# Performance work log

Measured on AMD Instinct MI355X. Metric: run time of the kernel, lower is better.

The kernel has to match this reference:

```python
import jax, jax.numpy as jnp
import numpy as np

BATCH = 256
SEQ_LEN = 96
PRED_LEN = 96
ENC_IN = 321
D_MODEL = 512


def setup_inputs() -> dict:
    key = jax.random.key(0)
    ks = jax.random.split(key, 7)
    s = 1.0 / np.sqrt(D_MODEL)
    x_enc = jax.random.normal(ks[0], (BATCH, SEQ_LEN, ENC_IN), jnp.float32)
    Wih = jax.random.uniform(ks[1], (4 * D_MODEL, ENC_IN), jnp.float32, -s, s)
    Whh = jax.random.uniform(ks[2], (4 * D_MODEL, D_MODEL), jnp.float32, -s, s)
    bih = jax.random.uniform(ks[3], (4 * D_MODEL,), jnp.float32, -s, s)
    bhh = jax.random.uniform(ks[4], (4 * D_MODEL,), jnp.float32, -s, s)
    Wp = jax.random.uniform(ks[5], (ENC_IN, D_MODEL), jnp.float32, -s, s)
    bp = jax.random.uniform(ks[6], (ENC_IN,), jnp.float32, -s, s)
    return {"x_enc": x_enc, "Wih": Wih, "Whh": Whh, "bih": bih, "bhh": bhh, "Wp": Wp, "bp": bp}


def _lstm_step(h, c, xt, Wih, Whh, bih, bhh):
    # PyTorch LSTM gate layout: [i, f, g, o]
    g = xt @ Wih.T + h @ Whh.T + (bih + bhh)  # (B, 4*D)
    i, f, gg, o = jnp.split(g, 4, axis=-1)
    c = jax.nn.sigmoid(f) * c + jax.nn.sigmoid(i) * jnp.tanh(gg)
    h = jax.nn.sigmoid(o) * jnp.tanh(c)
    return h, c


def reference(x_enc, Wih, Whh, bih, bhh, Wp, bp):
    # Instance norm over time (use_norm=True); means detached as in torch
    means = jax.lax.stop_gradient(jnp.mean(x_enc, axis=1, keepdims=True))
    xc = x_enc - means
    stdev = jnp.sqrt(jnp.var(xc, axis=1, keepdims=True) + 1e-5)
    x = xc / stdev

    B = x.shape[0]
    h0 = jnp.zeros((B, D_MODEL), x.dtype)
    c0 = jnp.zeros((B, D_MODEL), x.dtype)

    def enc_step(carry, xt):
        h, c = carry
        h, c = _lstm_step(h, c, xt, Wih, Whh, bih, bhh)
        return (h, c), None

    (h, c), _ = jax.lax.scan(enc_step, (h0, c0), jnp.swapaxes(x, 0, 1))

    def dec_step(carry, _):
        h, c = carry
        y = h @ Wp.T + bp          # (B, ENC_IN) decoded from hidden
        h, c = _lstm_step(h, c, y, Wih, Whh, bih, bhh)
        return (h, c), y

    _, ys = jax.lax.scan(dec_step, (h, c), None, length=PRED_LEN)
    dec_out = jnp.swapaxes(ys, 0, 1)  # (B, PRED_LEN, ENC_IN)

    dec_out = dec_out * stdev[:, 0:1, :] + means[:, 0:1, :]
    return dec_out
```

## Files before the change

kernel.cpp:

```cpp
#include <hip/hip_runtime.h>
#include <hip/hip_bf16.h>
#include <math.h>

#define BB 256
#define TT 96
#define PP 96
#define CC 321
#define CP 352
#define DD 512
#define GG 2048
#define NSTEPS 191

typedef __attribute__((ext_vector_type(8))) short bf16x8;
typedef __attribute__((ext_vector_type(4))) float f32x4;
typedef __hip_bfloat16 bf16;
typedef unsigned long long u64;

__global__ void norm_kernel(const float* __restrict__ x, float* __restrict__ meanp,
                            float* __restrict__ stdp, bf16* __restrict__ xn) {
    int g = blockIdx.x * 256 + threadIdx.x;
    if (g >= BB * CC) return;
    int b = g / CC, c = g % CC;
    const float* xp = x + b * TT * CC + c;
    float s = 0.f;
    for (int t = 0; t < TT; ++t) s += xp[t * CC];
    float mu = s * (1.f / TT);
    float v = 0.f;
    for (int t = 0; t < TT; ++t) { float d0 = xp[t * CC] - mu; v += d0 * d0; }
    float sd = sqrtf(v * (1.f / TT) + 1e-5f);
    float rs = 1.f / sd;
    meanp[g] = mu;
    stdp[g] = sd;
    for (int t = 0; t < TT; ++t)
        xn[(t * BB + b) * CP + c] = __float2bfloat16((xp[t * CC] - mu) * rs);
}

__global__ void cast_pad_kernel(const float* __restrict__ src, bf16* __restrict__ dst,
                                int rows, int cols, int ldd) {
    int i = blockIdx.x * 256 + threadIdx.x;
    if (i >= rows * cols) return;
    int r = i / cols, c = i % cols;
    dst[r * ldd + c] = __float2bfloat16(src[i]);
}

__global__ void transpose_wp_kernel(const float* __restrict__ wp, bf16* __restrict__ wpt) {
    int i = blockIdx.x * 256 + threadIdx.x;
    if (i >= DD * CC) return;
    int d = i / CC, c = i % CC;
    wpt[d * CP + c] = __float2bfloat16(wp[c * DD + d]);
}

__global__ void bias_kernel(const float* __restrict__ Wih, const float* __restrict__ bih,
                            const float* __restrict__ bhh, const float* __restrict__ bp,
                            float* __restrict__ bsum, float* __restrict__ beff) {
    int j = blockIdx.x * 256 + threadIdx.x;
    if (j >= GG) return;
    float s = bih[j] + bhh[j];
    float acc = 0.f;
    const float* w = Wih + j * CC;
    for (int c = 0; c < CC; ++c) acc += w[c] * bp[c];
    bsum[j] = s;
    beff[j] = s + acc;
}

__device__ __forceinline__ void gemm_core_64x64(const bf16* A, int lda, const bf16* Bt,
                                                int ldb, int K, int m0, int n0,
                                                f32x4 acc[4]) {
    __shared__ unsigned short As[64][40];
    __shared__ unsigned short Bs[64][40];
    int tid = threadIdx.x;
    int w = tid >> 6, lane = tid & 63;
    int quad = lane >> 4, col = lane & 15;
    int lr = tid >> 2, lc = (tid & 3) * 8;
    for (int k0 = 0; k0 < K; k0 += 32) {
        __syncthreads();
        *(uint4*)&As[lr][lc] = *(const uint4*)&A[(size_t)(m0 + lr) * lda + k0 + lc];
        *(uint4*)&Bs[lr][lc] = *(const uint4*)&Bt[(size_t)(n0 + lr) * ldb + k0 + lc];
        __syncthreads();
        bf16x8 a = *(const bf16x8*)&As[w * 16 + col][quad * 8];
#pragma unroll
        for (int nt = 0; nt < 4; ++nt) {
            bf16x8 bfr = *(const bf16x8*)&Bs[nt * 16 + col][quad * 8];
            acc[nt] = __builtin_amdgcn_mfma_f32_16x16x32_bf16(a, bfr, acc[nt], 0, 0, 0);
        }
    }
}

__global__ void weff_kernel(const bf16* __restrict__ WihP, const bf16* __restrict__ WpTP,
                            const float* __restrict__ Whh, bf16* __restrict__ WeffP) {
    f32x4 acc[4] = {{0,0,0,0},{0,0,0,0},{0,0,0,0},{0,0,0,0}};
    int m0 = blockIdx.y * 64, n0 = blockIdx.x * 64;
    gemm_core_64x64(WihP, CP, WpTP, CP, CP, m0, n0, acc);
    int tid = threadIdx.x, w = tid >> 6, lane = tid & 63;
    int quad = lane >> 4, col = lane & 15;
#pragma unroll
    for (int nt = 0; nt < 4; ++nt)
#pragma unroll
        for (int r = 0; r < 4; ++r) {
            int j = m0 + w * 16 + quad * 4 + r;
            int d = n0 + nt * 16 + col;
            WeffP[j * DD + d] = __float2bfloat16(acc[nt][r] + Whh[j * DD + d]);
        }
}

__global__ void proj_kernel(const bf16* __restrict__ Hdec, const bf16* __restrict__ WpP,
                            const float* __restrict__ bp, const float* __restrict__ stdp,
                            const float* __restrict__ meanp, float* __restrict__ out) {
    f32x4 acc[4] = {{0,0,0,0},{0,0,0,0},{0,0,0,0},{0,0,0,0}};
    int m0 = blockIdx.x * 64, n0 = blockIdx.y * 64;
    gemm_core_64x64(Hdec, DD, WpP, DD, DD, m0, n0, acc);
    int tid = threadIdx.x, w = tid >> 6, lane = tid & 63;
    int quad = lane >> 4, col = lane & 15;
#pragma unroll
    for (int nt = 0; nt < 4; ++nt) {
        int c = n0 + nt * 16 + col;
        if (c >= CC) continue;
        float bpc = bp[c];
#pragma unroll
        for (int r = 0; r < 4; ++r) {
            int row = m0 + w * 16 + quad * 4 + r;
            int t = row >> 8, b = row & 255;
            float y = acc[nt][r] + bpc;
            int sc = b * CC + c;
            out[(b * PP + t) * CC + c] = y * stdp[sc] + meanp[sc];
        }
    }
}

__global__ __launch_bounds__(128, 1) void lstm_persistent(
        const bf16* __restrict__ xn,
        const bf16* __restrict__ WihP,
        const bf16* __restrict__ WhhP,
        const bf16* __restrict__ WeffP,
        const float* __restrict__ bsum, const float* __restrict__ beff,
        bf16* __restrict__ hA, bf16* __restrict__ hB,
        bf16* __restrict__ Hdec,
        unsigned int* __restrict__ bar) {
    __shared__ unsigned short Whs[4 * 16 * 16 * 32];
    __shared__ unsigned short Wxs[4 * 11 * 16 * 32];

    const int tid = threadIdx.x;
    const int w = tid >> 6, lane = tid & 63;
    const int quad = lane >> 4, col = lane & 15;
    const int dt = blockIdx.x & 31;
    const int bt = blockIdx.x >> 5;
    const int d0 = dt * 16;
    const int b0 = bt * 32;
    const int batch = b0 + w * 16 + col;

    for (int i = tid; i < 64 * 44; i += 128) {
        int row = i / 44, c8 = i % 44;
        int gt = row >> 4, cl = row & 15;
        int ki = c8 >> 2, q = c8 & 3;
        *(uint4*)&Wxs[((gt * 11 + ki) * 16 + cl) * 32 + q * 8] =
            *((const uint4*)(WihP + (size_t)(gt * DD + d0 + cl) * CP) + c8);
    }
    for (int i = tid; i < 64 * 64; i += 128) {
        int row = i >> 6, c8 = i & 63;
        int gt = row >> 4, cl = row & 15;
        int ki = c8 >> 2, q = c8 & 3;
        *(uint4*)&Whs[((gt * 16 + ki) * 16 + cl) * 32 + q * 8] =
            *((const uint4*)(WhhP + (size_t)(gt * DD + d0 + cl) * DD) + c8);
    }
    __syncthreads();

    float creg[4] = {0.f, 0.f, 0.f, 0.f};
    float bs_[16], be_[16];
#pragma unroll
    for (int g4 = 0; g4 < 16; ++g4) {
        int gt = g4 >> 2, r = g4 & 3;
        bs_[g4] = bsum[gt * DD + d0 + quad * 4 + r];
        be_[g4] = beff[gt * DD + d0 + quad * 4 + r];
    }

    unsigned int gen = 0;

    for (int s = 0; s < NSTEPS; ++s) {
        const bool enc = (s < TT);
        const bf16* h_in;
        bf16* h_out;
        if (enc) {
            h_in  = (s & 1) ? hB : hA;
            h_out = (s == TT - 1) ? Hdec : ((s & 1) ? hA : hB);
        } else {
            int td = s - TT;
            h_in  = Hdec + (size_t)td * BB * DD;
            h_out = Hdec + (size_t)(td + 1) * BB * DD;
        }

        if (s == TT) {
            for (int i = tid; i < 64 * 64; i += 128) {
                int row = i >> 6, c8 = i & 63;
                int gt = row >> 4, cl = row & 15;
                int ki = c8 >> 2, q = c8 & 3;
                *(uint4*)&Whs[((gt * 16 + ki) * 16 + cl) * 32 + q * 8] =
                    *((const uint4*)(WeffP + (size_t)(gt * DD + d0 + cl) * DD) + c8);
            }
            __syncthreads();
        }

        f32x4 acc[4] = {{0,0,0,0},{0,0,0,0},{0,0,0,0},{0,0,0,0}};

        u64 hf[32];
        {
            u64* hp = (u64*)(h_in + (size_t)batch * DD);
#pragma unroll
            for (int ki = 0; ki < 16; ++ki) {
                hf[2 * ki] = __hip_atomic_load(&hp[ki * 8 + quad * 2],
                                               __ATOMIC_RELAXED, __HIP_MEMORY_SCOPE_AGENT);
                hf[2 * ki + 1] = __hip_atomic_load(&hp[ki * 8 + quad * 2 + 1],
                                                   __ATOMIC_RELAXED, __HIP_MEMORY_SCOPE_AGENT);
            }
        }

        if (enc) {
            uint4 xf[11];
            const uint4* xp = (const uint4*)(xn + (size_t)(s * BB + batch) * CP) + quad;
#pragma unroll
            for (int ki = 0; ki < 11; ++ki) xf[ki] = xp[ki * 4];
#pragma unroll
            for (int ki = 0; ki < 11; ++ki) {
                bf16x8 xv = *(bf16x8*)&xf[ki];
#pragma unroll
                for (int gt = 0; gt < 4; ++gt) {
                    bf16x8 wf = *(const bf16x8*)&Wxs[((gt * 11 + ki) * 16 + col) * 32 + quad * 8];
                    acc[gt] = __builtin_amdgcn_mfma_f32_16x16x32_bf16(wf, xv, acc[gt], 0, 0, 0);
                }
            }
        }

#pragma unroll
        for (int ki = 0; ki < 16; ++ki) {
            union { u64 q[2]; bf16x8 v; } hu;
            hu.q[0] = hf[2 * ki];
            hu.q[1] = hf[2 * ki + 1];
#pragma unroll
            for (int gt = 0; gt < 4; ++gt) {
                bf16x8 wf = *(const bf16x8*)&Whs[((gt * 16 + ki) * 16 + col) * 32 + quad * 8];
                acc[gt] = __builtin_amdgcn_mfma_f32_16x16x32_bf16(wf, hu.v, acc[gt], 0, 0, 0);
            }
        }

        u64 pack = 0;
#pragma unroll
        for (int r = 0; r < 4; ++r) {
            float iv = acc[0][r] + (enc ? bs_[0 + r] : be_[0 + r]);
            float fv = acc[1][r] + (enc ? bs_[4 + r] : be_[4 + r]);
            float gv = acc[2][r] + (enc ? bs_[8 + r] : be_[8 + r]);
            float ov = acc[3][r] + (enc ? bs_[12 + r] : be_[12 + r]);
            float si = 1.f / (1.f + __expf(-iv));
            float sf = 1.f / (1.f + __expf(-fv));
            float so = 1.f / (1.f + __expf(-ov));
            float tg = tanhf(gv);
            float cc = sf * creg[r] + si * tg;
            creg[r] = cc;
            float hv = so * tanhf(cc);
            union { bf16 h; unsigned short u; } cv;
            cv.h = __float2bfloat16(hv);
            pack |= (u64)cv.u << (16 * r);
        }
        __hip_atomic_store((u64*)&h_out[(size_t)batch * DD + d0 + quad * 4], pack,
                           __ATOMIC_RELAXED, __HIP_MEMORY_SCOPE_AGENT);

        if (s < NSTEPS - 1) {
            ++gen;
            __builtin_amdgcn_s_waitcnt(0);
            __syncthreads();
            if (tid == 0) {
                __hip_atomic_fetch_add(&bar[bt * 32], 1u, __ATOMIC_RELAXED,
                                       __HIP_MEMORY_SCOPE_AGENT);
                unsigned int tgt = gen * 32u;
                while (__hip_atomic_load(&bar[bt * 32], __ATOMIC_RELAXED,
                                         __HIP_MEMORY_SCOPE_AGENT) < tgt)
                    __builtin_amdgcn_s_sleep(1);
            }
            __syncthreads();
        }
    }
}

extern "C" void kernel_launch(void* const* d_in, const int* in_sizes, int n_in,
                              void* d_out, int out_size, void* d_ws, size_t ws_size,
                              hipStream_t stream) {
    (void)in_sizes; (void)n_in; (void)out_size;
    const float* x_enc = (const float*)d_in[0];
    const float* Wih   = (const float*)d_in[1];
    const float* Whh   = (const float*)d_in[2];
    const float* bih   = (const float*)d_in[3];
    const float* bhh   = (const float*)d_in[4];
    const float* Wp    = (const float*)d_in[5];
    const float* bp    = (const float*)d_in[6];
    float* out = (float*)d_out;

    char* ws = (char*)d_ws;
    size_t off = 0;
    float* meanp = (float*)(ws + off); off += (size_t)BB * CC * 4;
    float* stdp  = (float*)(ws + off); off += (size_t)BB * CC * 4;
    bf16* xnormP = (bf16*)(ws + off);  off += (size_t)TT * BB * CP * 2;
    bf16* WihP   = (bf16*)(ws + off);  off += (size_t)GG * CP * 2;
    bf16* WhhP   = (bf16*)(ws + off);  off += (size_t)GG * DD * 2;
    bf16* WeffP  = (bf16*)(ws + off);  off += (size_t)GG * DD * 2;
    bf16* WpTP   = (bf16*)(ws + off);  off += (size_t)DD * CP * 2;
    bf16* WpP    = (bf16*)(ws + off);  off += (size_t)384 * DD * 2;
    float* bsum  = (float*)(ws + off); off += (size_t)GG * 4;
    float* beff  = (float*)(ws + off); off += (size_t)GG * 4;
    bf16* hA     = (bf16*)(ws + off);  off += (size_t)BB * DD * 2;
    bf16* hB     = (bf16*)(ws + off);  off += (size_t)BB * DD * 2;
    bf16* Hdec   = (bf16*)(ws + off);  off += (size_t)PP * BB * DD * 2;
    unsigned int* bar = (unsigned int*)(ws + off); off += 1024;
    if (ws_size < off) return;

    hipMemsetAsync(xnormP, 0, (size_t)TT * BB * CP * 2, stream);
    hipMemsetAsync(WihP,   0, (size_t)GG * CP * 2, stream);
    hipMemsetAsync(WpTP,   0, (size_t)DD * CP * 2, stream);
    hipMemsetAsync(WpP,    0, (size_t)384 * DD * 2, stream);
    hipMemsetAsync(hA,     0, (size_t)BB * DD * 2, stream);
    hipMemsetAsync(bar,    0, 1024, stream);

    norm_kernel<<<(BB * CC + 255) / 256, 256, 0, stream>>>(x_enc, meanp, stdp, xnormP);
    cast_pad_kernel<<<(GG * CC + 255) / 256, 256, 0, stream>>>(Wih, WihP, GG, CC, CP);
    cast_pad_kernel<<<(GG * DD + 255) / 256, 256, 0, stream>>>(Whh, WhhP, GG, DD, DD);
    cast_pad_kernel<<<(CC * DD + 255) / 256, 256, 0, stream>>>(Wp, WpP, CC, DD, DD);
    transpose_wp_kernel<<<(DD * CC + 255) / 256, 256, 0, stream>>>(Wp, WpTP);
    bias_kernel<<<GG / 256, 256, 0, stream>>>(Wih, bih, bhh, bp, bsum, beff);
    weff_kernel<<<dim3(DD / 64, GG / 64), 256, 0, stream>>>(WihP, WpTP, Whh, WeffP);

    const bf16* xn_c = xnormP;  const bf16* wih_c = WihP;
    const bf16* whh_c = WhhP;   const bf16* weff_c = WeffP;
    const float* bs_c = bsum;   const float* be_c = beff;
    bf16* hA_c = hA; bf16* hB_c = hB; bf16* hd_c = Hdec; unsigned int* bar_c = bar;
    void* args[] = {&xn_c, &wih_c, &whh_c, &weff_c, &bs_c, &be_c,
                    &hA_c, &hB_c, &hd_c, &bar_c};
    hipLaunchCooperativeKernel((void*)lstm_persistent, dim3(256), dim3(128),
                               args, 0, stream);

    proj_kernel<<<dim3(PP * BB / 64, 384 / 64), 256, 0, stream>>>(
        Hdec, WpP, bp, stdp, meanp, out);
}
```

Before: 1.383 ms.

## Replace block barrier with per-wave flag sync and XCD-local batch tiles

```diff
diff --git a/kernel.cpp b/kernel.cpp
--- a/kernel.cpp
+++ b/kernel.cpp
@@ -136,31 +136,38 @@
         bf16* __restrict__ hA, bf16* __restrict__ hB,
         bf16* __restrict__ Hdec,
         unsigned int* __restrict__ bar) {
-    __shared__ unsigned short Whs[4 * 16 * 16 * 32];
-    __shared__ unsigned short Wxs[4 * 11 * 16 * 32];
+    __shared__ unsigned short Whs[4 * 16 * 64 * 8];
+    __shared__ unsigned short Wxs[4 * 11 * 64 * 8];
+    __shared__ int role_sh;
 
     const int tid = threadIdx.x;
     const int w = tid >> 6, lane = tid & 63;
     const int quad = lane >> 4, col = lane & 15;
-    const int dt = blockIdx.x & 31;
-    const int bt = blockIdx.x >> 5;
+
+    unsigned int xcd;
+    asm volatile("s_getreg_b32 %0, hwreg(HW_REG_XCC_ID)" : "=s"(xcd));
+    xcd &= 7;
+    if (tid == 0)
+        role_sh = (int)__hip_atomic_fetch_add(&bar[xcd], 1u, __ATOMIC_RELAXED,
+                                              __HIP_MEMORY_SCOPE_AGENT);
+    __syncthreads();
+    const int dt = role_sh & 31;
+    const int bt = (int)xcd;
     const int d0 = dt * 16;
     const int b0 = bt * 32;
     const int batch = b0 + w * 16 + col;
-
-    for (int i = tid; i < 64 * 44; i += 128) {
-        int row = i / 44, c8 = i % 44;
-        int gt = row >> 4, cl = row & 15;
-        int ki = c8 >> 2, q = c8 & 3;
-        *(uint4*)&Wxs[((gt * 11 + ki) * 16 + cl) * 32 + q * 8] =
-            *((const uint4*)(WihP + (size_t)(gt * DD + d0 + cl) * CP) + c8);
-    }
-    for (int i = tid; i < 64 * 64; i += 128) {
-        int row = i >> 6, c8 = i & 63;
-        int gt = row >> 4, cl = row & 15;
-        int ki = c8 >> 2, q = c8 & 3;
-        *(uint4*)&Whs[((gt * 16 + ki) * 16 + cl) * 32 + q * 8] =
-            *((const uint4*)(WhhP + (size_t)(gt * DD + d0 + cl) * DD) + c8);
+    unsigned int* const flags = bar + 64 + bt * 64;
+
+    for (int i = tid; i < 4096; i += 128) {
+        int q = i & 3, ki = (i >> 2) & 15, row = (i >> 6) & 15, gt = i >> 10;
+        *(uint4*)&Whs[((gt * 16 + ki) * 64 + q * 16 + row) * 8] =
+            *(const uint4*)&WhhP[(size_t)(gt * DD + d0 + row) * DD + ki * 32 + q * 8];
+    }
+    for (int i = tid; i < 2816; i += 128) {
+        int q = i & 3; int t = i >> 2; int ki = t % 11; t /= 11;
+        int row = t & 15, gt = t >> 4;
+        *(uint4*)&Wxs[((gt * 11 + ki) * 64 + q * 16 + row) * 8] =
+            *(const uint4*)&WihP[(size_t)(gt * DD + d0 + row) * CP + ki * 32 + q * 8];
     }
     __syncthreads();
 
@@ -172,8 +179,6 @@
         bs_[g4] = bsum[gt * DD + d0 + quad * 4 + r];
         be_[g4] = beff[gt * DD + d0 + quad * 4 + r];
     }
-
-    unsigned int gen = 0;
 
     for (int s = 0; s < NSTEPS; ++s) {
         const bool enc = (s < TT);
@@ -188,18 +193,43 @@
             h_out = Hdec + (size_t)(td + 1) * BB * DD;
         }
 
+        f32x4 acc[4] = {{0,0,0,0},{0,0,0,0},{0,0,0,0},{0,0,0,0}};
+
+        if (enc) {
+            uint4 xf[11];
+            const uint4* xp = (const uint4*)(xn + (size_t)(s * BB + batch) * CP) + quad;
+#pragma unroll
+            for (int ki = 0; ki < 11; ++ki) xf[ki] = xp[ki * 4];
+#pragma unroll
+            for (int ki = 0; ki < 11; ++ki) {
+                bf16x8 xv = *(bf16x8*)&xf[ki];
+#pragma unroll
+                for (int gt = 0; gt < 4; ++gt) {
+                    bf16x8 wf = *(const bf16x8*)&Wxs[((gt * 11 + ki) * 64 + lane) * 8];
+                    acc[gt] = __builtin_amdgcn_mfma_f32_16x16x32_bf16(wf, xv, acc[gt], 0, 0, 0);
+                }
+            }
+        }
+
+        if (s > 0) {
+            unsigned int tgt = (unsigned int)s;
+            unsigned int v;
+            int guard = 0;
+            do {
+                v = __hip_atomic_load(&flags[lane], __ATOMIC_RELAXED,
+                                      __HIP_MEMORY_SCOPE_AGENT);
+            } while (v < tgt && ++guard < (1 << 22));
+            __builtin_amdgcn_sched_barrier(0);
+        }
+
         if (s == TT) {
-            for (int i = tid; i < 64 * 64; i += 128) {
-                int row = i >> 6, c8 = i & 63;
-                int gt = row >> 4, cl = row & 15;
-                int ki = c8 >> 2, q = c8 & 3;
-                *(uint4*)&Whs[((gt * 16 + ki) * 16 + cl) * 32 + q * 8] =
-                    *((const uint4*)(WeffP + (size_t)(gt * DD + d0 + cl) * DD) + c8);
+            for (int i = tid; i < 4096; i += 128) {
+                int q = i & 3, ki = (i >> 2) & 15, row = (i >> 6) & 15, gt = i >> 10;
+                *(uint4*)&Whs[((gt * 16 + ki) * 64 + q * 16 + row) * 8] =
+                    *(const uint4*)&WeffP[(size_t)(gt * DD + d0 + row) * DD + ki * 32 + q * 8];
             }
             __syncthreads();
         }
-
-        f32x4 acc[4] = {{0,0,0,0},{0,0,0,0},{0,0,0,0},{0,0,0,0}};
 
         u64 hf[32];
         {
@@ -213,22 +243,6 @@
             }
         }
 
-        if (enc) {
-            uint4 xf[11];
-            const uint4* xp = (const uint4*)(xn + (size_t)(s * BB + batch) * CP) + quad;
-#pragma unroll
-            for (int ki = 0; ki < 11; ++ki) xf[ki] = xp[ki * 4];
-#pragma unroll
-            for (int ki = 0; ki < 11; ++ki) {
-                bf16x8 xv = *(bf16x8*)&xf[ki];
-#pragma unroll
-                for (int gt = 0; gt < 4; ++gt) {
-                    bf16x8 wf = *(const bf16x8*)&Wxs[((gt * 11 + ki) * 16 + col) * 32 + quad * 8];
-                    acc[gt] = __builtin_amdgcn_mfma_f32_16x16x32_bf16(wf, xv, acc[gt], 0, 0, 0);
-                }
-            }
-        }
-
 #pragma unroll
         for (int ki = 0; ki < 16; ++ki) {
             union { u64 q[2]; bf16x8 v; } hu;
@@ -236,7 +250,7 @@
             hu.q[1] = hf[2 * ki + 1];
 #pragma unroll
             for (int gt = 0; gt < 4; ++gt) {
-                bf16x8 wf = *(const bf16x8*)&Whs[((gt * 16 + ki) * 16 + col) * 32 + quad * 8];
+                bf16x8 wf = *(const bf16x8*)&Whs[((gt * 16 + ki) * 64 + lane) * 8];
                 acc[gt] = __builtin_amdgcn_mfma_f32_16x16x32_bf16(wf, hu.v, acc[gt], 0, 0, 0);
             }
         }
@@ -254,28 +268,17 @@
             float tg = tanhf(gv);
             float cc = sf * creg[r] + si * tg;
             creg[r] = cc;
-            float hv = so * tanhf(cc);
+            float hvv = so * tanhf(cc);
             union { bf16 h; unsigned short u; } cv;
-            cv.h = __float2bfloat16(hv);
+            cv.h = __float2bfloat16(hvv);
             pack |= (u64)cv.u << (16 * r);
         }
         __hip_atomic_store((u64*)&h_out[(size_t)batch * DD + d0 + quad * 4], pack,
                            __ATOMIC_RELAXED, __HIP_MEMORY_SCOPE_AGENT);
-
-        if (s < NSTEPS - 1) {
-            ++gen;
-            __builtin_amdgcn_s_waitcnt(0);
-            __syncthreads();
-            if (tid == 0) {
-                __hip_atomic_fetch_add(&bar[bt * 32], 1u, __ATOMIC_RELAXED,
-                                       __HIP_MEMORY_SCOPE_AGENT);
-                unsigned int tgt = gen * 32u;
-                while (__hip_atomic_load(&bar[bt * 32], __ATOMIC_RELAXED,
-                                         __HIP_MEMORY_SCOPE_AGENT) < tgt)
-                    __builtin_amdgcn_s_sleep(1);
-            }
-            __syncthreads();
-        }
+        asm volatile("s_waitcnt vmcnt(0)" ::: "memory");
+        if (lane == 0)
+            __hip_atomic_store(&flags[dt * 2 + w], (unsigned int)(s + 1),
+                               __ATOMIC_RELAXED, __HIP_MEMORY_SCOPE_AGENT);
     }
 }
 
@@ -307,7 +310,7 @@
     bf16* hA     = (bf16*)(ws + off);  off += (size_t)BB * DD * 2;
     bf16* hB     = (bf16*)(ws + off);  off += (size_t)BB * DD * 2;
     bf16* Hdec   = (bf16*)(ws + off);  off += (size_t)PP * BB * DD * 2;
-    unsigned int* bar = (unsigned int*)(ws + off); off += 1024;
+    unsigned int* bar = (unsigned int*)(ws + off); off += 4096;
     if (ws_size < off) return;
 
     hipMemsetAsync(xnormP, 0, (size_t)TT * BB * CP * 2, stream);
@@ -315,7 +318,7 @@
     hipMemsetAsync(WpTP,   0, (size_t)DD * CP * 2, stream);
     hipMemsetAsync(WpP,    0, (size_t)384 * DD * 2, stream);
     hipMemsetAsync(hA,     0, (size_t)BB * DD * 2, stream);
-    hipMemsetAsync(bar,    0, 1024, stream);
+    hipMemsetAsync(bar,    0, 4096, stream);
 
     norm_kernel<<<(BB * CC + 255) / 256, 256, 0, stream>>>(x_enc, meanp, stdp, xnormP);
     cast_pad_kernel<<<(GG * CC + 255) / 256, 256, 0, stream>>>(Wih, WihP, GG, CC, CP);
```

Measured after the change: 1.569 ms. 1.13x slower.
